# Optimization experiments

Measured on AMD Instinct MI355X. Metric: run time of the kernel, lower is better.

## Reference

```python
import jax, jax.numpy as jnp
import numpy as np

N_NODES = 100000
N_EDGES = 1600000
N_GRAPHS = 2048
F_IN = 33
D = 256


def _graph_conv(x, edge_index, w_rel, b_rel, w_root):
    # PyG GraphConv (aggr='add'): out = lin_rel(sum_j x_j) + lin_root(x)
    src, dst = edge_index[0], edge_index[1]
    agg = jax.ops.segment_sum(x[src], dst, num_segments=x.shape[0])  # [N, F]
    return agg @ w_rel + b_rel + x @ w_root


def setup_inputs() -> dict:
    key = jax.random.key(0)
    ks = jax.random.split(key, 16)
    scale_in = 1.0 / np.sqrt(F_IN)
    scale_d = 1.0 / np.sqrt(D)
    inp = {
        "x": jax.random.normal(ks[0], (N_NODES, F_IN), dtype=jnp.float32),
        "edge_index": jax.random.randint(ks[1], (2, N_EDGES), 0, N_NODES),
        "batch_index": jnp.sort(jax.random.randint(ks[2], (N_NODES,), 0, N_GRAPHS)),
        # initial_conv: GraphConv(F_IN -> D)
        "w_rel0": jax.random.normal(ks[3], (F_IN, D), dtype=jnp.float32) * scale_in,
        "b_rel0": jnp.zeros((D,), dtype=jnp.float32),
        "w_root0": jax.random.normal(ks[4], (F_IN, D), dtype=jnp.float32) * scale_in,
        # conv1..conv3: GraphConv(D -> D)
        "w_rel1": jax.random.normal(ks[5], (D, D), dtype=jnp.float32) * scale_d,
        "b_rel1": jnp.zeros((D,), dtype=jnp.float32),
        "w_root1": jax.random.normal(ks[6], (D, D), dtype=jnp.float32) * scale_d,
        "w_rel2": jax.random.normal(ks[7], (D, D), dtype=jnp.float32) * scale_d,
        "b_rel2": jnp.zeros((D,), dtype=jnp.float32),
        "w_root2": jax.random.normal(ks[8], (D, D), dtype=jnp.float32) * scale_d,
        "w_rel3": jax.random.normal(ks[9], (D, D), dtype=jnp.float32) * scale_d,
        "b_rel3": jnp.zeros((D,), dtype=jnp.float32),
        "w_root3": jax.random.normal(ks[10], (D, D), dtype=jnp.float32) * scale_d,
        # output head Linear(D -> 1)
        "w_out": jax.random.normal(ks[11], (D, 1), dtype=jnp.float32) * scale_d,
        "b_out": jnp.zeros((1,), dtype=jnp.float32),
    }
    return inp


def reference(x, edge_index, batch_index,
              w_rel0, b_rel0, w_root0,
              w_rel1, b_rel1, w_root1,
              w_rel2, b_rel2, w_root2,
              w_rel3, b_rel3, w_root3,
              w_out, b_out):
    # dropout omitted (eval mode)
    h = jax.nn.gelu(_graph_conv(x, edge_index, w_rel0, b_rel0, w_root0))
    h = jax.nn.gelu(_graph_conv(h, edge_index, w_rel1, b_rel1, w_root1))
    h = jax.nn.gelu(_graph_conv(h, edge_index, w_rel2, b_rel2, w_root2))
    h = jax.nn.gelu(_graph_conv(h, edge_index, w_rel3, b_rel3, w_root3))
    # global mean pool over graphs
    sums = jax.ops.segment_sum(h, batch_index, num_segments=N_GRAPHS)          # [G, D]
    counts = jax.ops.segment_sum(jnp.ones((h.shape[0],), h.dtype), batch_index,
                                 num_segments=N_GRAPHS)                         # [G]
    pooled = sums / jnp.maximum(counts, 1.0)[:, None]
    return pooled @ w_out + b_out                                               # [G, 1]
```

## Files before the change

### kernel.cpp

```cpp
#include <hip/hip_runtime.h>
#include <math.h>

#define NN 100000
#define NE 1600000
#define NG 2048
#define FIN 33
#define DD 256

#define SH 8
#define NB ((NN + 255) >> 8)
#define CH 4096
#define PCAP 4608
#define ESCAP 6144

typedef __attribute__((ext_vector_type(8))) short bf16x8;
typedef __attribute__((ext_vector_type(4))) float f32x4;

__device__ __forceinline__ float b2f(unsigned short u){
    union { unsigned int i; float f; } c; c.i = ((unsigned int)u) << 16; return c.f;
}
__device__ __forceinline__ unsigned short f2b(float f){
    union { float f; unsigned int u; } c; c.f = f;
    unsigned int r = c.u + 0x7fffu + ((c.u >> 16) & 1u);
    return (unsigned short)(r >> 16);
}

__device__ __forceinline__ float gelu_tanh(float x){
    float x3 = x * x * x;
    float t = tanhf(0.7978845608028654f * (x + 0.044715f * x3));
    return 0.5f * x * (1.0f + t);
}

__global__ __launch_bounds__(256) void k_bin(const int* __restrict__ src,
                                             const int* __restrict__ dst,
                                             int* __restrict__ gcur,
                                             int2* __restrict__ pairs){
    __shared__ int cnt[NB];
    __shared__ int lb[NB];
    __shared__ int gbase[NB];
    __shared__ int sc[512];
    __shared__ int2 stage[CH];

    int t = threadIdx.x;
    for(int i = t; i < NB; i += 256) cnt[i] = 0;
    __syncthreads();

    int e0 = blockIdx.x * CH;
    int n = NE - e0; if(n > CH) n = CH;

    int  myb[16];
    int  myr[16];
    int2 myp[16];
    #pragma unroll
    for(int k = 0; k < 16; k++){
        int e = e0 + t + k * 256;
        if(e < NE){
            int s = src[e], d = dst[e];
            int b = d >> SH;
            myr[k] = atomicAdd(&cnt[b], 1);
            myb[k] = b;
            myp[k] = make_int2(s, d);
        } else myb[k] = -1;
    }
    __syncthreads();

    sc[t]       = (t       < NB) ? cnt[t]       : 0;
    sc[t + 256] = (t + 256 < NB) ? cnt[t + 256] : 0;
    __syncthreads();
    for(int off = 1; off < 512; off <<= 1){
        int a  = (t >= off)       ? sc[t - off]       : 0;
        int b2 = (t + 256 >= off) ? sc[t + 256 - off] : 0;
        __syncthreads();
        sc[t] += a; sc[t + 256] += b2;
        __syncthreads();
    }
    for(int i = t; i < NB; i += 256){
        lb[i] = sc[i] - cnt[i];
        int c = cnt[i];
        gbase[i] = (c > 0) ? atomicAdd(&gcur[i], c) : 0;
    }
    __syncthreads();

    #pragma unroll
    for(int k = 0; k < 16; k++){
        if(myb[k] >= 0) stage[lb[myb[k]] + myr[k]] = myp[k];
    }
    __syncthreads();

    for(int i = t; i < n; i += 256){
        int2 p = stage[i];
        int b = p.y >> SH;
        int tgt = gbase[b] + (i - lb[b]);
        if(tgt < PCAP) pairs[(size_t)b * PCAP + tgt] = p;
    }
}

__global__ void k_sscan(const int* __restrict__ gcur, int* __restrict__ boff){
    __shared__ int s[512];
    int t = threadIdx.x;
    int v = 0;
    if(t < NB){ v = gcur[t]; if(v > PCAP) v = PCAP; }
    s[t] = v; __syncthreads();
    for(int off = 1; off < 512; off <<= 1){
        int u = (t >= off) ? s[t - off] : 0;
        __syncthreads();
        s[t] += u;
        __syncthreads();
    }
    if(t < NB) boff[t] = s[t] - v;
}

__global__ __launch_bounds__(256) void k_bcsr(const int2* __restrict__ pairs,
                                              const int* __restrict__ gcur,
                                              const int* __restrict__ boff,
                                              int* __restrict__ deg,
                                              int* __restrict__ rs,
                                              int* __restrict__ esrc){
    __shared__ int hist[256];
    __shared__ int sc[256];
    __shared__ int cur2[256];
    __shared__ int est[ESCAP];

    int b = blockIdx.x;
    int t = threadIdx.x;
    int m = gcur[b]; if(m > PCAP) m = PCAP;
    int pstart = boff[b];
    const int2* bp = pairs + (size_t)b * PCAP;

    hist[t] = 0;
    __syncthreads();
    for(int i = t; i < m; i += 256) atomicAdd(&hist[bp[i].y & 255], 1);
    __syncthreads();

    sc[t] = hist[t]; __syncthreads();
    for(int off = 1; off < 256; off <<= 1){
        int u = (t >= off) ? sc[t - off] : 0;
        __syncthreads();
        sc[t] += u;
        __syncthreads();
    }
    int excl = sc[t] - hist[t];
    cur2[t] = excl;
    int node = (b << 8) + t;
    if(node < NN){
        deg[node] = hist[t];
        rs[node]  = pstart + excl;
    }
    __syncthreads();

    for(int i = t; i < m; i += 256){
        int2 p = bp[i];
        int pos = atomicAdd(&cur2[p.y & 255], 1);
        if(pos < ESCAP) est[pos] = p.x;
        else esrc[pstart + pos] = p.x;
    }
    __syncthreads();
    int lim = (m < ESCAP) ? m : ESCAP;
    for(int i = t; i < lim; i += 256) esrc[pstart + i] = est[i];
}

__global__ void k_xpad(const float* __restrict__ x, unsigned short* __restrict__ xb){
    int idx = blockIdx.x * 256 + threadIdx.x;
    if(idx >= NN * 64) return;
    int n = idx >> 6, c = idx & 63;
    xb[idx] = (c < FIN) ? f2b(x[(size_t)n * FIN + c]) : 0;
}

__global__ void k_aggx(const unsigned short* __restrict__ xb, const int* __restrict__ rs,
                       const int* __restrict__ deg, const int* __restrict__ esrc,
                       unsigned short* __restrict__ axb){
    int wv = (blockIdx.x * blockDim.x + threadIdx.x) >> 6;
    int lane = threadIdx.x & 63;
    int node = wv * 4 + (lane >> 4);
    int l16 = lane & 15;
    if(node >= NN) return;
    int start = rs[node], cnt = deg[node];
    float a0 = 0.f, a1 = 0.f, a2 = 0.f, a3 = 0.f;
    const unsigned short* xp = xb + l16 * 4;
    int j = 0;
    for(; j + 4 <= cnt; j += 4){
        int e0 = esrc[start+j], e1 = esrc[start+j+1], e2 = esrc[start+j+2], e3 = esrc[start+j+3];
        ushort4 v0 = *(const ushort4*)(xp + (size_t)e0 * 64);
        ushort4 v1 = *(const ushort4*)(xp + (size_t)e1 * 64);
        ushort4 v2 = *(const ushort4*)(xp + (size_t)e2 * 64);
        ushort4 v3 = *(const ushort4*)(xp + (size_t)e3 * 64);
        a0 += (b2f(v0.x) + b2f(v1.x)) + (b2f(v2.x) + b2f(v3.x));
        a1 += (b2f(v0.y) + b2f(v1.y)) + (b2f(v2.y) + b2f(v3.y));
        a2 += (b2f(v0.z) + b2f(v1.z)) + (b2f(v2.z) + b2f(v3.z));
        a3 += (b2f(v0.w) + b2f(v1.w)) + (b2f(v2.w) + b2f(v3.w));
    }
    for(; j < cnt; j++){
        int e = esrc[start + j];
        ushort4 v = *(const ushort4*)(xp + (size_t)e * 64);
        a0 += b2f(v.x); a1 += b2f(v.y); a2 += b2f(v.z); a3 += b2f(v.w);
    }
    ushort4 o; o.x = f2b(a0); o.y = f2b(a1); o.z = f2b(a2); o.w = f2b(a3);
    *(ushort4*)(axb + (size_t)node * 64 + l16 * 4) = o;
}

__global__ void k_agg256(const unsigned short* __restrict__ h, const int* __restrict__ rs,
                         const int* __restrict__ deg, const int* __restrict__ esrc,
                         unsigned short* __restrict__ agg){
    int wv = (blockIdx.x * blockDim.x + threadIdx.x) >> 6;
    int lane = threadIdx.x & 63;
    int node = wv * 2 + (lane >> 5);
    int l32 = lane & 31;
    if(node >= NN) return;
    int start = rs[node], cnt = deg[node];
    float a[8] = {0.f,0.f,0.f,0.f,0.f,0.f,0.f,0.f};
    const unsigned short* hp = h + l32 * 8;
    int j = 0;
    for(; j + 8 <= cnt; j += 8){
        bf16x8 v[8];
        #pragma unroll
        for(int q = 0; q < 8; q++){
            int e = esrc[start + j + q];
            v[q] = *(const bf16x8*)(hp + (size_t)e * DD);
        }
        #pragma unroll
        for(int q = 0; q < 8; q++)
            #pragma unroll
            for(int d = 0; d < 8; d++)
                a[d] += b2f((unsigned short)v[q][d]);
    }
    for(; j < cnt; j++){
        int e = esrc[start + j];
        bf16x8 v = *(const bf16x8*)(hp + (size_t)e * DD);
        #pragma unroll
        for(int d = 0; d < 8; d++) a[d] += b2f((unsigned short)v[d]);
    }
    bf16x8 o;
    #pragma unroll
    for(int d = 0; d < 8; d++) o[d] = (short)f2b(a[d]);
    *(bf16x8*)(agg + (size_t)node * DD + l32 * 8) = o;
}

__global__ void k_wt(const float* __restrict__ W, unsigned short* __restrict__ Bt){
    __shared__ float s[16][17];
    int tx = threadIdx.x, ty = threadIdx.y;
    int k = blockIdx.y * 16 + ty;
    int j = blockIdx.x * 16 + tx;
    s[ty][tx] = W[k * DD + j];
    __syncthreads();
    Bt[(size_t)(blockIdx.x * 16 + ty) * DD + blockIdx.y * 16 + tx] = f2b(s[tx][ty]);
}

__global__ void k_wt0(const float* __restrict__ W, unsigned short* __restrict__ Bt){
    int idx = blockIdx.x * 256 + threadIdx.x;
    if(idx >= DD * 64) return;
    int j = idx >> 6, k = idx & 63;
    Bt[idx] = (k < FIN) ? f2b(W[(size_t)k * DD + j]) : 0;
}

#define BMM 128
#define BNN 128
#define LPAD 40

template<int KS, int AST>
__global__ __launch_bounds__(256) void k_mfma_gemm(
    const unsigned short* __restrict__ A0, const unsigned short* __restrict__ A1,
    const unsigned short* __restrict__ Bt0, const unsigned short* __restrict__ Bt1,
    const float* __restrict__ bias, unsigned short* __restrict__ out)
{
    __shared__ unsigned short As[2][BMM * LPAD];
    __shared__ unsigned short Bs[2][BNN * LPAD];

    int t = threadIdx.x;
    int lane = t & 63;
    int w = t >> 6;
    int wm = (w >> 1) * 64;
    int wn = (w & 1) * 64;
    int i0 = blockIdx.x * BMM;
    int j0 = blockIdx.y * BNN;

    int r16 = lane & 15;
    int kg  = lane >> 4;

    int srow0 = t >> 2,          sseg0 = (t & 3) * 8;
    int srow1 = (t + 256) >> 2,  sseg1 = ((t + 256) & 3) * 8;

    f32x4 acc[4][4];
    #pragma unroll
    for(int m = 0; m < 4; m++)
        #pragma unroll
        for(int n = 0; n < 4; n++)
            acc[m][n] = (f32x4){0.f, 0.f, 0.f, 0.f};

    const int steps = 2 * KS;

    auto loadStep = [&](int s, bf16x8* va, bf16x8* vb){
        const unsigned short* Ap = (s < KS) ? A0 : A1;
        const unsigned short* Bp = (s < KS) ? Bt0 : Bt1;
        int kk = ((s < KS) ? s : s - KS) * 32;
        int gi0 = i0 + srow0, gi1 = i0 + srow1;
        va[0] = (bf16x8){};
        va[1] = (bf16x8){};
        if(gi0 < NN) va[0] = *(const bf16x8*)(Ap + (size_t)gi0 * AST + kk + sseg0);
        if(gi1 < NN) va[1] = *(const bf16x8*)(Ap + (size_t)gi1 * AST + kk + sseg1);
        vb[0] = *(const bf16x8*)(Bp + (size_t)(j0 + srow0) * AST + kk + sseg0);
        vb[1] = *(const bf16x8*)(Bp + (size_t)(j0 + srow1) * AST + kk + sseg1);
    };
    auto writeStep = [&](int buf, const bf16x8* va, const bf16x8* vb){
        *(bf16x8*)(&As[buf][srow0 * LPAD + sseg0]) = va[0];
        *(bf16x8*)(&As[buf][srow1 * LPAD + sseg1]) = va[1];
        *(bf16x8*)(&Bs[buf][srow0 * LPAD + sseg0]) = vb[0];
        *(bf16x8*)(&Bs[buf][srow1 * LPAD + sseg1]) = vb[1];
    };

    bf16x8 va[2], vb[2], va2[2], vb2[2];
    loadStep(0, va, vb);
    writeStep(0, va, vb);
    int cur = 0;

    for(int s = 0; s < steps; s++){
        bool more = (s + 1 < steps);
        if(more) loadStep(s + 1, va2, vb2);
        __syncthreads();

        bf16x8 af[4], bfr[4];
        #pragma unroll
        for(int m = 0; m < 4; m++)
            af[m] = *(const bf16x8*)(&As[cur][(wm + m * 16 + r16) * LPAD + kg * 8]);
        #pragma unroll
        for(int n = 0; n < 4; n++)
            bfr[n] = *(const bf16x8*)(&Bs[cur][(wn + n * 16 + r16) * LPAD + kg * 8]);
        #pragma unroll
        for(int m = 0; m < 4; m++)
            #pragma unroll
            for(int n = 0; n < 4; n++)
                acc[m][n] = __builtin_amdgcn_mfma_f32_16x16x32_bf16(af[m], bfr[n], acc[m][n], 0, 0, 0);

        if(more) writeStep(cur ^ 1, va2, vb2);
        cur ^= 1;
    }

    int rg = kg * 4;
    #pragma unroll
    for(int n = 0; n < 4; n++){
        int gj = j0 + wn + n * 16 + r16;
        float bb = bias[gj];
        #pragma unroll
        for(int m = 0; m < 4; m++){
            #pragma unroll
            for(int r = 0; r < 4; r++){
                int gi = i0 + wm + m * 16 + rg + r;
                if(gi < NN)
                    out[(size_t)gi * DD + gj] = f2b(gelu_tanh(acc[m][n][r] + bb));
            }
        }
    }
}

__global__ void k_pool(const unsigned short* __restrict__ h, const int* __restrict__ batch,
                       const float* __restrict__ wout, float* __restrict__ gsum,
                       int* __restrict__ gcnt){
    int w = (blockIdx.x * blockDim.x + threadIdx.x) >> 6;
    int lane = threadIdx.x & 63;
    if(w >= NN) return;
    ushort4 hv = *(const ushort4*)(h + (size_t)w * DD + lane * 4);
    float4 wv = *(const float4*)(wout + lane * 4);
    float d = b2f(hv.x)*wv.x + b2f(hv.y)*wv.y + b2f(hv.z)*wv.z + b2f(hv.w)*wv.w;
    for(int off = 32; off > 0; off >>= 1) d += __shfl_down(d, off);
    if(lane == 0){
        int g = batch[w];
        atomicAdd(&gsum[g], d);
        atomicAdd(&gcnt[g], 1);
    }
}

__global__ void k_final(const float* __restrict__ gsum, const int* __restrict__ gcnt,
                        const float* __restrict__ bout, float* __restrict__ out){
    int g = blockIdx.x * 256 + threadIdx.x;
    if(g < NG) out[g] = gsum[g] / fmaxf((float)gcnt[g], 1.f) + bout[0];
}

extern "C" void kernel_launch(void* const* d_in, const int* in_sizes, int n_in,
                              void* d_out, int out_size, void* d_ws, size_t ws_size,
                              hipStream_t stream){
    const float* x       = (const float*)d_in[0];
    const int*   ei      = (const int*)d_in[1];
    const int*   src     = ei;
    const int*   dst     = ei + NE;
    const int*   batch   = (const int*)d_in[2];
    const float* w_rel0  = (const float*)d_in[3];
    const float* b_rel0  = (const float*)d_in[4];
    const float* w_root0 = (const float*)d_in[5];
    const float* w_rel1  = (const float*)d_in[6];
    const float* b_rel1  = (const float*)d_in[7];
    const float* w_root1 = (const float*)d_in[8];
    const float* w_rel2  = (const float*)d_in[9];
    const float* b_rel2  = (const float*)d_in[10];
    const float* w_root2 = (const float*)d_in[11];
    const float* w_rel3  = (const float*)d_in[12];
    const float* b_rel3  = (const float*)d_in[13];
    const float* w_root3 = (const float*)d_in[14];
    const float* w_out   = (const float*)d_in[15];
    const float* b_out   = (const float*)d_in[16];
    float* out = (float*)d_out;

    char* ws = (char*)d_ws;
    size_t off = 0;
    auto alloc = [&](size_t bytes) -> void* {
        void* p = ws + off;
        off = (off + bytes + 255) & ~(size_t)255;
        return p;
    };
    unsigned short* hA  = (unsigned short*)alloc((size_t)NN * DD * 2);
    unsigned short* hB  = (unsigned short*)alloc((size_t)NN * DD * 2);
    unsigned short* agg = (unsigned short*)alloc((size_t)NN * DD * 2);
    int*   deg  = (int*)alloc((size_t)NN * 4);
    int*   rs   = (int*)alloc((size_t)NN * 4);
    int*   esrc = (int*)alloc((size_t)NE * 4);
    int*   gcur = (int*)alloc(512 * 4);
    int*   boff = (int*)alloc(512 * 4);
    float* gsum = (float*)alloc((size_t)NG * 4);
    int*   gcnt = (int*)alloc((size_t)NG * 4);
    unsigned short* bt[6];
    for(int i = 0; i < 6; i++) bt[i] = (unsigned short*)alloc((size_t)DD * DD * 2);
    unsigned short* bt0r = (unsigned short*)alloc((size_t)DD * 64 * 2);
    unsigned short* bt0o = (unsigned short*)alloc((size_t)DD * 64 * 2);
    (void)ws_size; (void)in_sizes; (void)n_in; (void)out_size;

    int2* pairs = (int2*)hB;
    unsigned short* xb  = agg;
    unsigned short* axb = agg + (size_t)NN * 64 + 128;

    hipMemsetAsync(gcur, 0, 512 * 4, stream);
    k_bin<<<(NE + CH - 1) / CH, 256, 0, stream>>>(src, dst, gcur, pairs);
    k_sscan<<<1, 512, 0, stream>>>(gcur, boff);
    k_bcsr<<<NB, 256, 0, stream>>>(pairs, gcur, boff, deg, rs, esrc);

    dim3 wtg(16, 16), wtb(16, 16);
    k_wt<<<wtg, wtb, 0, stream>>>(w_rel1,  bt[0]);
    k_wt<<<wtg, wtb, 0, stream>>>(w_root1, bt[1]);
    k_wt<<<wtg, wtb, 0, stream>>>(w_rel2,  bt[2]);
    k_wt<<<wtg, wtb, 0, stream>>>(w_root2, bt[3]);
    k_wt<<<wtg, wtb, 0, stream>>>(w_rel3,  bt[4]);
    k_wt<<<wtg, wtb, 0, stream>>>(w_root3, bt[5]);
    k_wt0<<<(DD * 64 + 255) / 256, 256, 0, stream>>>(w_rel0,  bt0r);
    k_wt0<<<(DD * 64 + 255) / 256, 256, 0, stream>>>(w_root0, bt0o);
    k_xpad<<<(NN * 64 + 255) / 256, 256, 0, stream>>>(x, xb);

    int aggGrid  = (NN + 3) / 4;
    int agg2Grid = (NN * 32 + 255) / 256;
    dim3 gg((NN + BMM - 1) / BMM, DD / BNN);

    k_aggx<<<(NN + 15) / 16, 256, 0, stream>>>(xb, rs, deg, esrc, axb);
    k_mfma_gemm<2, 64><<<gg, 256, 0, stream>>>(axb, xb, bt0r, bt0o, b_rel0, hA);
    k_agg256<<<agg2Grid, 256, 0, stream>>>(hA, rs, deg, esrc, agg);
    k_mfma_gemm<8, 256><<<gg, 256, 0, stream>>>(agg, hA, bt[0], bt[1], b_rel1, hB);
    k_agg256<<<agg2Grid, 256, 0, stream>>>(hB, rs, deg, esrc, agg);
    k_mfma_gemm<8, 256><<<gg, 256, 0, stream>>>(agg, hB, bt[2], bt[3], b_rel2, hA);
    k_agg256<<<agg2Grid, 256, 0, stream>>>(hA, rs, deg, esrc, agg);
    k_mfma_gemm<8, 256><<<gg, 256, 0, stream>>>(agg, hA, bt[4], bt[5], b_rel3, hB);

    hipMemsetAsync(gsum, 0, (size_t)NG * 4, stream);
    hipMemsetAsync(gcnt, 0, (size_t)NG * 4, stream);
    k_pool<<<aggGrid, 256, 0, stream>>>(hB, batch, w_out, gsum, gcnt);
    k_final<<<(NG + 255) / 256, 256, 0, stream>>>(gsum, gcnt, b_out, out);
}
```

Baseline: 910.7 us.

## Restructure GEMM to keep full-K weight slice in LDS and stream A from registers

The GEMM now loads a 64-column slice of both weight matrices for the entire K into shared memory once per block. Each of 8 waves then streams its own 32 rows of A directly from global memory into registers, double-buffered, so the per-step LDS staging and barriers for A are gone. Blocks use 512 threads and a swizzled 1D grid so the four column-slice blocks for a group of row tiles are launched close together and can share A through cache. The costs are that each A row is read from global/L2 by four separate blocks, and for K=512 the weight slice takes about 66 KB of LDS, which limits occupancy.

```diff
diff --git a/kernel.cpp b/kernel.cpp
--- a/kernel.cpp
+++ b/kernel.cpp
@@ -12,6 +12,8 @@
 #define CH 4096
 #define PCAP 4608
 #define ESCAP 6144
+
+#define RBLKS ((NN + 255) / 256)
 
 typedef __attribute__((ext_vector_type(8))) short bf16x8;
 typedef __attribute__((ext_vector_type(4))) float f32x4;
@@ -252,98 +254,90 @@
     Bt[idx] = (k < FIN) ? f2b(W[(size_t)k * DD + j]) : 0;
 }
 
-#define BMM 128
-#define BNN 128
-#define LPAD 40
-
 template<int KS, int AST>
-__global__ __launch_bounds__(256) void k_mfma_gemm(
+__global__ __launch_bounds__(512, 4) void k_mfma_gemm(
     const unsigned short* __restrict__ A0, const unsigned short* __restrict__ A1,
     const unsigned short* __restrict__ Bt0, const unsigned short* __restrict__ Bt1,
     const float* __restrict__ bias, unsigned short* __restrict__ out)
 {
-    __shared__ unsigned short As[2][BMM * LPAD];
-    __shared__ unsigned short Bs[2][BNN * LPAD];
+    constexpr int KHALF = KS * 32;
+    constexpr int KTOT  = 2 * KHALF;
+    constexpr int BST   = KTOT + 8;
+    __shared__ unsigned short Bs[64 * BST];
 
     int t = threadIdx.x;
     int lane = t & 63;
     int w = t >> 6;
-    int wm = (w >> 1) * 64;
-    int wn = (w & 1) * 64;
-    int i0 = blockIdx.x * BMM;
-    int j0 = blockIdx.y * BNN;
-
     int r16 = lane & 15;
     int kg  = lane >> 4;
 
-    int srow0 = t >> 2,          sseg0 = (t & 3) * 8;
-    int srow1 = (t + 256) >> 2,  sseg1 = ((t + 256) & 3) * 8;
-
-    f32x4 acc[4][4];
-    #pragma unroll
-    for(int m = 0; m < 4; m++)
+    int bid = blockIdx.x;
+    int rblk = (bid >> 5) * 8 + (bid & 7);
+    int j0p  = (bid >> 3) & 3;
+    if(rblk >= RBLKS) return;
+    int i0 = rblk * 256;
+    int jbase = j0p * 64;
+
+    constexpr int SEG = KTOT / 8;
+    #pragma unroll
+    for(int p = 0; p < (64 * SEG) / 512; p++){
+        int idx = p * 512 + t;
+        int row = idx / SEG;
+        int k = (idx % SEG) * 8;
+        bf16x8 v;
+        if(k < KHALF) v = *(const bf16x8*)(Bt0 + (size_t)(jbase + row) * AST + k);
+        else          v = *(const bf16x8*)(Bt1 + (size_t)(jbase + row) * AST + (k - KHALF));
+        *(bf16x8*)(&Bs[row * BST + k]) = v;
+    }
+    __syncthreads();
+
+    int baseRow = i0 + w * 32;
+    auto loadA = [&](int ks, bf16x8* af){
+        const unsigned short* Ap = (ks < KS) ? A0 : A1;
+        int kk = ((ks < KS) ? ks : ks - KS) * 32 + kg * 8;
+        #pragma unroll
+        for(int m = 0; m < 2; m++){
+            int gi = baseRow + m * 16 + r16;
+            if(gi > NN - 1) gi = NN - 1;
+            af[m] = *(const bf16x8*)(Ap + (size_t)gi * AST + kk);
+        }
+    };
+
+    f32x4 acc[2][4];
+    #pragma unroll
+    for(int m = 0; m < 2; m++)
         #pragma unroll
         for(int n = 0; n < 4; n++)
             acc[m][n] = (f32x4){0.f, 0.f, 0.f, 0.f};
 
-    const int steps = 2 * KS;
-
-    auto loadStep = [&](int s, bf16x8* va, bf16x8* vb){
-        const unsigned short* Ap = (s < KS) ? A0 : A1;
-        const unsigned short* Bp = (s < KS) ? Bt0 : Bt1;
-        int kk = ((s < KS) ? s : s - KS) * 32;
-        int gi0 = i0 + srow0, gi1 = i0 + srow1;
-        va[0] = (bf16x8){};
-        va[1] = (bf16x8){};
-        if(gi0 < NN) va[0] = *(const bf16x8*)(Ap + (size_t)gi0 * AST + kk + sseg0);
-        if(gi1 < NN) va[1] = *(const bf16x8*)(Ap + (size_t)gi1 * AST + kk + sseg1);
-        vb[0] = *(const bf16x8*)(Bp + (size_t)(j0 + srow0) * AST + kk + sseg0);
-        vb[1] = *(const bf16x8*)(Bp + (size_t)(j0 + srow1) * AST + kk + sseg1);
-    };
-    auto writeStep = [&](int buf, const bf16x8* va, const bf16x8* vb){
-        *(bf16x8*)(&As[buf][srow0 * LPAD + sseg0]) = va[0];
-        *(bf16x8*)(&As[buf][srow1 * LPAD + sseg1]) = va[1];
-        *(bf16x8*)(&Bs[buf][srow0 * LPAD + sseg0]) = vb[0];
-        *(bf16x8*)(&Bs[buf][srow1 * LPAD + sseg1]) = vb[1];
-    };
-
-    bf16x8 va[2], vb[2], va2[2], vb2[2];
-    loadStep(0, va, vb);
-    writeStep(0, va, vb);
-    int cur = 0;
-
-    for(int s = 0; s < steps; s++){
-        bool more = (s + 1 < steps);
-        if(more) loadStep(s + 1, va2, vb2);
-        __syncthreads();
-
-        bf16x8 af[4], bfr[4];
-        #pragma unroll
-        for(int m = 0; m < 4; m++)
-            af[m] = *(const bf16x8*)(&As[cur][(wm + m * 16 + r16) * LPAD + kg * 8]);
+    bf16x8 afb[2][2];
+    loadA(0, afb[0]);
+    loadA(1, afb[1]);
+
+    #pragma unroll
+    for(int ks = 0; ks < 2 * KS; ks++){
+        bf16x8 bfr[4];
         #pragma unroll
         for(int n = 0; n < 4; n++)
-            bfr[n] = *(const bf16x8*)(&Bs[cur][(wn + n * 16 + r16) * LPAD + kg * 8]);
-        #pragma unroll
-        for(int m = 0; m < 4; m++)
+            bfr[n] = *(const bf16x8*)(&Bs[(n * 16 + r16) * BST + ks * 32 + kg * 8]);
+        #pragma unroll
+        for(int m = 0; m < 2; m++)
             #pragma unroll
             for(int n = 0; n < 4; n++)
-                acc[m][n] = __builtin_amdgcn_mfma_f32_16x16x32_bf16(af[m], bfr[n], acc[m][n], 0, 0, 0);
-
-        if(more) writeStep(cur ^ 1, va2, vb2);
-        cur ^= 1;
+                acc[m][n] = __builtin_amdgcn_mfma_f32_16x16x32_bf16(afb[ks & 1][m], bfr[n], acc[m][n], 0, 0, 0);
+        if(ks + 2 < 2 * KS) loadA(ks + 2, afb[ks & 1]);
     }
 
     int rg = kg * 4;
     #pragma unroll
     for(int n = 0; n < 4; n++){
-        int gj = j0 + wn + n * 16 + r16;
+        int gj = jbase + n * 16 + r16;
         float bb = bias[gj];
         #pragma unroll
-        for(int m = 0; m < 4; m++){
+        for(int m = 0; m < 2; m++){
             #pragma unroll
             for(int r = 0; r < 4; r++){
-                int gi = i0 + wm + m * 16 + rg + r;
+                int gi = baseRow + m * 16 + rg + r;
                 if(gi < NN)
                     out[(size_t)gi * DD + gj] = f2b(gelu_tanh(acc[m][n][r] + bb));
             }
@@ -443,16 +437,16 @@
 
     int aggGrid  = (NN + 3) / 4;
     int agg2Grid = (NN * 32 + 255) / 256;
-    dim3 gg((NN + BMM - 1) / BMM, DD / BNN);
+    int gemmGrid = ((RBLKS + 7) / 8) * 32;
 
     k_aggx<<<(NN + 15) / 16, 256, 0, stream>>>(xb, rs, deg, esrc, axb);
-    k_mfma_gemm<2, 64><<<gg, 256, 0, stream>>>(axb, xb, bt0r, bt0o, b_rel0, hA);
+    k_mfma_gemm<2, 64><<<gemmGrid, 512, 0, stream>>>(axb, xb, bt0r, bt0o, b_rel0, hA);
     k_agg256<<<agg2Grid, 256, 0, stream>>>(hA, rs, deg, esrc, agg);
-    k_mfma_gemm<8, 256><<<gg, 256, 0, stream>>>(agg, hA, bt[0], bt[1], b_rel1, hB);
+    k_mfma_gemm<8, 256><<<gemmGrid, 512, 0, stream>>>(agg, hA, bt[0], bt[1], b_rel1, hB);
     k_agg256<<<agg2Grid, 256, 0, stream>>>(hB, rs, deg, esrc, agg);
-    k_mfma_gemm<8, 256><<<gg, 256, 0, stream>>>(agg, hB, bt[2], bt[3], b_rel2, hA);
+    k_mfma_gemm<8, 256><<<gemmGrid, 512, 0, stream>>>(agg, hB, bt[2], bt[3], b_rel2, hA);
     k_agg256<<<agg2Grid, 256, 0, stream>>>(hA, rs, deg, esrc, agg);
-    k_mfma_gemm<8, 256><<<gg, 256, 0, stream>>>(agg, hA, bt[4], bt[5], b_rel3, hB);
+    k_mfma_gemm<8, 256><<<gemmGrid, 512, 0, stream>>>(agg, hA, bt[4], bt[5], b_rel3, hB);
 
     hipMemsetAsync(gsum, 0, (size_t)NG * 4, stream);
     hipMemsetAsync(gcnt, 0, (size_t)NG * 4, stream);
```

Result: faster. 821.8 us (-9.8%).
